# Kernel optimization log

Measured on AMD Instinct MI355X. Metric: run time of the kernel, lower is better.

The kernel has to match this reference:

```python
import jax, jax.numpy as jnp
import numpy as np


def setup_inputs() -> dict:
    key = jax.random.key(0)
    k1, k2 = jax.random.split(key)
    B, H, N, D = 4, 16, 2048, 64
    x = jax.random.normal(k1, (B, H, N, D), dtype=jnp.float32)
    wqkv = 0.02 * jax.random.normal(k2, (H, D, 3 * D), dtype=jnp.float32)
    bqkv = jnp.zeros((H, 1, 3 * D), dtype=jnp.float32)
    return {"x": x, "wqkv": wqkv, "bqkv": bqkv}


def reference(x, wqkv, bqkv):
    # x: [B, H, N, D]; wqkv: [H, D, 3D]; bqkv: [H, 1, 3D]
    B, H, N, D = x.shape
    scale = D ** (-0.5)
    qkv = jnp.einsum('bhnd,hde->bhne', x, wqkv) + bqkv  # [B,H,N,3D]
    # Faithful to torch: reshape (3D,) -> (D, 3) then unbind last axis,
    # i.e. q/k/v are interleaved (stride-3) columns of the projection.
    qkv = qkv.reshape(B, H, N, D, 3)
    q = qkv[..., 0] * scale
    k = qkv[..., 1]
    v = qkv[..., 2]
    attn = jnp.einsum('bhqd,bhkd->bhqk', q, k)  # [B,H,N,N]
    attn = jax.nn.softmax(attn, axis=-1)
    out = jnp.einsum('bhqk,bhkd->bhqd', attn, v)  # [B,H,N,D]
    return out
```

## Files before the change

kernel.cpp:

```cpp
#include <hip/hip_runtime.h>
#include <hip/hip_bf16.h>
#include <stdint.h>

typedef short bf16x8 __attribute__((ext_vector_type(8)));
typedef short bf16x4 __attribute__((ext_vector_type(4)));
typedef float f32x4 __attribute__((ext_vector_type(4)));

#define BHC 64
#define NQ 2048
#define DD 64
#define NE 192
#define LDP 72
#define WPS (64 * LDP + 8)
#define QSCALE 0.1803368801111245f

__device__ __forceinline__ short f2bf(float f) {
  unsigned u = __float_as_uint(f);
  unsigned r = (u + 0x7FFFu + ((u >> 16) & 1u)) >> 16;
  return (short)r;
}

__device__ __forceinline__ bf16x8 pack8(float4 a, float4 b) {
  bf16x8 v;
  v[0] = f2bf(a.x); v[1] = f2bf(a.y); v[2] = f2bf(a.z); v[3] = f2bf(a.w);
  v[4] = f2bf(b.x); v[5] = f2bf(b.y); v[6] = f2bf(b.z); v[7] = f2bf(b.w);
  return v;
}

__device__ __forceinline__ short2 pk_bf16(float a, float b) {
  __hip_bfloat162 c = __float22bfloat162_rn(make_float2(a, b));
  return *reinterpret_cast<short2*>(&c);
}

__global__ __launch_bounds__(256, 4) void proj_kernel(
    const float* __restrict__ x, const float* __restrict__ w,
    const float* __restrict__ bq, short* __restrict__ Qg,
    short* __restrict__ Kg, short* __restrict__ Vtg) {
  __shared__ short wt[3 * WPS];
  __shared__ short sV[4][64 * 24];

  const int tid = threadIdx.x;
  const int bh = blockIdx.x >> 5;
  const int rb = blockIdx.x & 31;
  const int h = bh & 15;

  const float* whp = w + (size_t)h * DD * NE;
  for (int i = 0; i < 48; ++i) {
    int idx = i * 256 + tid;
    int d = idx / NE, e = idx - d * NE;
    int dd = e / 3, wh = e - dd * 3;
    wt[wh * WPS + dd * LDP + d] = f2bf(whp[idx]);
  }
  __syncthreads();

  const int wave = tid >> 6;
  const int lane = tid & 63;
  const int col = lane & 15, quad = lane >> 4;
  const int row0 = rb * 64 + wave * 16;

  const float* xrow = x + ((size_t)bh * NQ + row0 + col) * DD;
  bf16x8 aq[2];
#pragma unroll
  for (int kc = 0; kc < 2; ++kc) {
    const float4* p4 = (const float4*)(xrow + kc * 32 + quad * 8);
    aq[kc] = pack8(p4[0], p4[1]);
  }

  f32x4 acc[12];
#pragma unroll
  for (int nt = 0; nt < 12; ++nt) acc[nt] = (f32x4){0.f, 0.f, 0.f, 0.f};

#pragma unroll
  for (int nt = 0; nt < 12; ++nt) {
    const short* wrow = &wt[(nt >> 2) * WPS + ((nt & 3) * 16 + col) * LDP];
#pragma unroll
    for (int kc = 0; kc < 2; ++kc) {
      bf16x8 bw = *(const bf16x8*)(wrow + kc * 32 + quad * 8);
      acc[nt] = __builtin_amdgcn_mfma_f32_16x16x32_bf16(aq[kc], bw, acc[nt], 0, 0, 0);
    }
  }

  const float* bqh = bq + h * NE;
  short* Qp = Qg + ((size_t)bh * NQ + row0) * DD;
  short* Kp = Kg + ((size_t)bh * NQ + row0) * DD;
  short* sVw = sV[wave];

#pragma unroll
  for (int nt = 0; nt < 12; ++nt) {
    int dd = (nt & 3) * 16 + col;
    float bias = bqh[dd * 3 + (nt >> 2)];
    float v0 = acc[nt][0] + bias, v1 = acc[nt][1] + bias;
    float v2 = acc[nt][2] + bias, v3 = acc[nt][3] + bias;
    if (nt < 4) { v0 *= QSCALE; v1 *= QSCALE; v2 *= QSCALE; v3 *= QSCALE; }
    short2 s01 = pk_bf16(v0, v1);
    short2 s23 = pk_bf16(v2, v3);
    int rowl = quad * 4;
    if (nt < 4) {
      Qp[rowl * DD + dd] = s01.x; Qp[(rowl + 1) * DD + dd] = s01.y;
      Qp[(rowl + 2) * DD + dd] = s23.x; Qp[(rowl + 3) * DD + dd] = s23.y;
    } else if (nt < 8) {
      Kp[rowl * DD + dd] = s01.x; Kp[(rowl + 1) * DD + dd] = s01.y;
      Kp[(rowl + 2) * DD + dd] = s23.x; Kp[(rowl + 3) * DD + dd] = s23.y;
    } else {
      sVw[dd * 24 + rowl] = s01.x; sVw[dd * 24 + rowl + 1] = s01.y;
      sVw[dd * 24 + rowl + 2] = s23.x; sVw[dd * 24 + rowl + 3] = s23.y;
    }
  }

  short* Vp = Vtg + (size_t)bh * DD * NQ + row0;
#pragma unroll
  for (int c = 0; c < 2; ++c) {
    int idx = c * 64 + lane;
    int d = idx >> 1, half = (idx & 1) * 8;
    *(bf16x8*)(Vp + (size_t)d * NQ + half) = *(const bf16x8*)(sVw + d * 24 + half);
  }
}

__global__ __launch_bounds__(256, 2) void attn_kernel(
    const short* __restrict__ Qg, const short* __restrict__ Kg,
    const short* __restrict__ Vtg, float* __restrict__ out) {
  __shared__ short kbuf[2][64 * 64];
  __shared__ short vbuf[2][64 * 64];
  __shared__ short pbuf[4][64 * LDP];

  const int tid = threadIdx.x;
  const int bh = blockIdx.x & 63;
  const int qb = blockIdx.x >> 6;
  const int wave = tid >> 6, lane = tid & 63;
  const int col = lane & 15, quad = lane >> 4;
  const int qbase = qb * 256 + wave * 64;

  bf16x8 bqf[4][2];
#pragma unroll
  for (int ntq = 0; ntq < 4; ++ntq)
#pragma unroll
    for (int kc = 0; kc < 2; ++kc)
      bqf[ntq][kc] = *(const bf16x8*)(Qg + ((size_t)bh * NQ + qbase + ntq * 16 + col) * DD +
                                      kc * 32 + quad * 8);

  f32x4 o[4][4];
  float l_acc[4];
#pragma unroll
  for (int mtq = 0; mtq < 4; ++mtq) {
    l_acc[mtq] = 0.f;
#pragma unroll
    for (int ntd = 0; ntd < 4; ++ntd) o[mtq][ntd] = (f32x4){0.f, 0.f, 0.f, 0.f};
  }

  short* pb = pbuf[wave];
  const short* Kb = Kg + (size_t)bh * NQ * DD;
  const short* Vb = Vtg + (size_t)bh * DD * NQ;

  const int r0 = tid >> 3, c0 = tid & 7;
  const int dst0 = r0 * 64 + ((c0 ^ (r0 & 7)) * 8);
  const int dst1 = (r0 + 32) * 64 + ((c0 ^ (r0 & 7)) * 8);
  const int src0 = r0 * DD + c0 * 8;
  const size_t vsrc0o = (size_t)r0 * NQ + c0 * 8;
  const size_t vsrc1o = (size_t)(r0 + 32) * NQ + c0 * 8;

  {
    bf16x8 k0 = *(const bf16x8*)(Kb + src0);
    bf16x8 k1 = *(const bf16x8*)(Kb + src0 + 32 * DD);
    bf16x8 v0 = *(const bf16x8*)(Vb + vsrc0o);
    bf16x8 v1 = *(const bf16x8*)(Vb + vsrc1o);
    *(bf16x8*)(&kbuf[0][dst0]) = k0;
    *(bf16x8*)(&kbuf[0][dst1]) = k1;
    *(bf16x8*)(&vbuf[0][dst0]) = v0;
    *(bf16x8*)(&vbuf[0][dst1]) = v1;
  }
  __syncthreads();

#pragma unroll 1
  for (int t = 0; t < 32; ++t) {
    const int p = t & 1;
    const short* kb = kbuf[p];
    const short* vb_s = vbuf[p];

    bf16x8 nk0, nk1, nv0, nv1;
    if (t < 31) {
      const short* Kn = Kb + (t + 1) * 64 * DD;
      const short* Vn = Vb + (t + 1) * 64;
      nk0 = *(const bf16x8*)(Kn + src0);
      nk1 = *(const bf16x8*)(Kn + src0 + 32 * DD);
      nv0 = *(const bf16x8*)(Vn + vsrc0o);
      nv1 = *(const bf16x8*)(Vn + vsrc1o);
    }

#pragma unroll
    for (int mtk = 0; mtk < 4; ++mtk) {
      const int krow = mtk * 16 + col;
      const int kx = krow & 7;
      bf16x8 ka0 = *(const bf16x8*)(&kb[krow * 64 + ((quad ^ kx) * 8)]);
      bf16x8 ka1 = *(const bf16x8*)(&kb[krow * 64 + (((4 + quad) ^ kx) * 8)]);
#pragma unroll
      for (int ntq = 0; ntq < 4; ++ntq) {
        f32x4 s = (f32x4){0.f, 0.f, 0.f, 0.f};
        s = __builtin_amdgcn_mfma_f32_16x16x32_bf16(ka0, bqf[ntq][0], s, 0, 0, 0);
        s = __builtin_amdgcn_mfma_f32_16x16x32_bf16(ka1, bqf[ntq][1], s, 0, 0, 0);
        float p0 = __builtin_amdgcn_exp2f(s[0]);
        float p1 = __builtin_amdgcn_exp2f(s[1]);
        float p2 = __builtin_amdgcn_exp2f(s[2]);
        float p3 = __builtin_amdgcn_exp2f(s[3]);
        l_acc[ntq] += (p0 + p1) + (p2 + p3);
        short2 s01 = pk_bf16(p0, p1);
        short2 s23 = pk_bf16(p2, p3);
        bf16x4 pv; pv[0] = s01.x; pv[1] = s01.y; pv[2] = s23.x; pv[3] = s23.y;
        *(bf16x4*)(&pb[(ntq * 16 + col) * LDP + mtk * 16 + quad * 4]) = pv;
      }
    }

#pragma unroll
    for (int mtq = 0; mtq < 4; ++mtq) {
      bf16x8 ap0 = *(const bf16x8*)(&pb[(mtq * 16 + col) * LDP + quad * 8]);
      bf16x8 ap1 = *(const bf16x8*)(&pb[(mtq * 16 + col) * LDP + 32 + quad * 8]);
#pragma unroll
      for (int ntd = 0; ntd < 4; ++ntd) {
        const int vrow = ntd * 16 + col;
        const int vx = vrow & 7;
        bf16x8 vf0 = *(const bf16x8*)(&vb_s[vrow * 64 + ((quad ^ vx) * 8)]);
        bf16x8 vf1 = *(const bf16x8*)(&vb_s[vrow * 64 + (((4 + quad) ^ vx) * 8)]);
        o[mtq][ntd] = __builtin_amdgcn_mfma_f32_16x16x32_bf16(ap0, vf0, o[mtq][ntd], 0, 0, 0);
        o[mtq][ntd] = __builtin_amdgcn_mfma_f32_16x16x32_bf16(ap1, vf1, o[mtq][ntd], 0, 0, 0);
      }
    }

    if (t < 31) {
      short* kn = kbuf[1 - p];
      short* vn = vbuf[1 - p];
      *(bf16x8*)(&kn[dst0]) = nk0;
      *(bf16x8*)(&kn[dst1]) = nk1;
      *(bf16x8*)(&vn[dst0]) = nv0;
      *(bf16x8*)(&vn[dst1]) = nv1;
      __syncthreads();
    }
  }

#pragma unroll
  for (int mtq = 0; mtq < 4; ++mtq) {
    float l = l_acc[mtq];
    l += __shfl_xor(l, 16);
    l += __shfl_xor(l, 32);
#pragma unroll
    for (int r = 0; r < 4; ++r) {
      float inv = 1.0f / __shfl(l, quad * 4 + r);
      int rq = qbase + mtq * 16 + quad * 4 + r;
      float* orow = out + ((size_t)bh * NQ + rq) * DD;
#pragma unroll
      for (int ntd = 0; ntd < 4; ++ntd) orow[ntd * 16 + col] = o[mtq][ntd][r] * inv;
    }
  }
}

extern "C" void kernel_launch(void* const* d_in, const int* in_sizes, int n_in,
                              void* d_out, int out_size, void* d_ws, size_t ws_size,
                              hipStream_t stream) {
  const float* x = (const float*)d_in[0];
  const float* w = (const float*)d_in[1];
  const float* bq = (const float*)d_in[2];
  float* out = (float*)d_out;

  short* Qg = (short*)d_ws;
  short* Kg = Qg + (size_t)BHC * NQ * DD;
  short* Vtg = Kg + (size_t)BHC * NQ * DD;

  proj_kernel<<<dim3(2048), dim3(256), 0, stream>>>(x, w, bq, Qg, Kg, Vtg);
  attn_kernel<<<dim3(512), dim3(256), 0, stream>>>(Qg, Kg, Vtg, out);
}
```

Measured before the change: 178.5 us.

## Pre-pack projection weights in MFMA fragment order via separate prep kernel

Adds a small kernel that converts the per-head QKV weights to bf16 once, already arranged in MFMA fragment order, and de-interleaves the bias. The projection kernel then loads weight fragments straight from global memory (L2-resident) instead of having each of 2048 blocks convert the full weight matrix into shared memory and synchronise. MFMA operands are swapped so each lane holds whole rows, which allows vectorized bf16x4 stores of Q and K. The cost is one extra kernel launch and weight reads from global or cache inside the MFMA loop rather than from LDS.

```diff
diff --git a/kernel.cpp b/kernel.cpp
--- a/kernel.cpp
+++ b/kernel.cpp
@@ -11,7 +11,6 @@
 #define DD 64
 #define NE 192
 #define LDP 72
-#define WPS (64 * LDP + 8)
 #define QSCALE 0.1803368801111245f
 
 __device__ __forceinline__ short f2bf(float f) {
@@ -32,27 +31,34 @@
   return *reinterpret_cast<short2*>(&c);
 }
 
+__global__ __launch_bounds__(256) void wprep_kernel(
+    const float* __restrict__ w, const float* __restrict__ bq,
+    short* __restrict__ wp, float* __restrict__ biasp) {
+  const int h = blockIdx.y;
+  const int r = blockIdx.x * 256 + threadIdx.x;
+  const int j = r & 7;
+  const int t = r >> 3;
+  const int quad = t & 3, col = (t >> 2) & 15;
+  const int kc = (t >> 6) & 1, ntb = (t >> 7) & 3, wh = t >> 9;
+  const int d = kc * 32 + quad * 8 + j;
+  const int e = (ntb * 16 + col) * 3 + wh;
+  wp[h * 12288 + r] = f2bf(w[((size_t)h * DD + d) * NE + e]);
+  if (r < 192) {
+    const int wh2 = r / 64, c = r - wh2 * 64;
+    biasp[h * 192 + r] = bq[h * NE + c * 3 + wh2];
+  }
+}
+
 __global__ __launch_bounds__(256, 4) void proj_kernel(
-    const float* __restrict__ x, const float* __restrict__ w,
-    const float* __restrict__ bq, short* __restrict__ Qg,
+    const float* __restrict__ x, const short* __restrict__ wp,
+    const float* __restrict__ biasp, short* __restrict__ Qg,
     short* __restrict__ Kg, short* __restrict__ Vtg) {
-  __shared__ short wt[3 * WPS];
   __shared__ short sV[4][64 * 24];
 
   const int tid = threadIdx.x;
   const int bh = blockIdx.x >> 5;
   const int rb = blockIdx.x & 31;
   const int h = bh & 15;
-
-  const float* whp = w + (size_t)h * DD * NE;
-  for (int i = 0; i < 48; ++i) {
-    int idx = i * 256 + tid;
-    int d = idx / NE, e = idx - d * NE;
-    int dd = e / 3, wh = e - dd * 3;
-    wt[wh * WPS + dd * LDP + d] = f2bf(whp[idx]);
-  }
-  __syncthreads();
-
   const int wave = tid >> 6;
   const int lane = tid & 63;
   const int col = lane & 15, quad = lane >> 4;
@@ -66,44 +72,45 @@
     aq[kc] = pack8(p4[0], p4[1]);
   }
 
+  const short* wph = wp + h * 12288;
+  const int fo = (col * 4 + quad) * 8;
+
   f32x4 acc[12];
 #pragma unroll
   for (int nt = 0; nt < 12; ++nt) acc[nt] = (f32x4){0.f, 0.f, 0.f, 0.f};
 
 #pragma unroll
   for (int nt = 0; nt < 12; ++nt) {
-    const short* wrow = &wt[(nt >> 2) * WPS + ((nt & 3) * 16 + col) * LDP];
-#pragma unroll
-    for (int kc = 0; kc < 2; ++kc) {
-      bf16x8 bw = *(const bf16x8*)(wrow + kc * 32 + quad * 8);
-      acc[nt] = __builtin_amdgcn_mfma_f32_16x16x32_bf16(aq[kc], bw, acc[nt], 0, 0, 0);
-    }
-  }
-
-  const float* bqh = bq + h * NE;
-  short* Qp = Qg + ((size_t)bh * NQ + row0) * DD;
-  short* Kp = Kg + ((size_t)bh * NQ + row0) * DD;
+    bf16x8 bw0 = *(const bf16x8*)(wph + (nt * 2 + 0) * 512 + fo);
+    bf16x8 bw1 = *(const bf16x8*)(wph + (nt * 2 + 1) * 512 + fo);
+    acc[nt] = __builtin_amdgcn_mfma_f32_16x16x32_bf16(bw0, aq[0], acc[nt], 0, 0, 0);
+    acc[nt] = __builtin_amdgcn_mfma_f32_16x16x32_bf16(bw1, aq[1], acc[nt], 0, 0, 0);
+  }
+
+  const float* bph = biasp + h * 192;
+  short* Qp = Qg + ((size_t)bh * NQ + row0 + col) * DD;
+  short* Kp = Kg + ((size_t)bh * NQ + row0 + col) * DD;
   short* sVw = sV[wave];
 
 #pragma unroll
   for (int nt = 0; nt < 12; ++nt) {
-    int dd = (nt & 3) * 16 + col;
-    float bias = bqh[dd * 3 + (nt >> 2)];
-    float v0 = acc[nt][0] + bias, v1 = acc[nt][1] + bias;
-    float v2 = acc[nt][2] + bias, v3 = acc[nt][3] + bias;
+    const int wh = nt >> 2, ntb = nt & 3;
+    const float4 b4 = *(const float4*)(bph + wh * 64 + ntb * 16 + quad * 4);
+    float v0 = acc[nt][0] + b4.x, v1 = acc[nt][1] + b4.y;
+    float v2 = acc[nt][2] + b4.z, v3 = acc[nt][3] + b4.w;
     if (nt < 4) { v0 *= QSCALE; v1 *= QSCALE; v2 *= QSCALE; v3 *= QSCALE; }
-    short2 s01 = pk_bf16(v0, v1);
-    short2 s23 = pk_bf16(v2, v3);
-    int rowl = quad * 4;
-    if (nt < 4) {
-      Qp[rowl * DD + dd] = s01.x; Qp[(rowl + 1) * DD + dd] = s01.y;
-      Qp[(rowl + 2) * DD + dd] = s23.x; Qp[(rowl + 3) * DD + dd] = s23.y;
-    } else if (nt < 8) {
-      Kp[rowl * DD + dd] = s01.x; Kp[(rowl + 1) * DD + dd] = s01.y;
-      Kp[(rowl + 2) * DD + dd] = s23.x; Kp[(rowl + 3) * DD + dd] = s23.y;
+    if (nt < 8) {
+      short2 s01 = pk_bf16(v0, v1);
+      short2 s23 = pk_bf16(v2, v3);
+      bf16x4 pv; pv[0] = s01.x; pv[1] = s01.y; pv[2] = s23.x; pv[3] = s23.y;
+      short* P = (nt < 4) ? Qp : Kp;
+      *(bf16x4*)(P + ntb * 16 + quad * 4) = pv;
     } else {
-      sVw[dd * 24 + rowl] = s01.x; sVw[dd * 24 + rowl + 1] = s01.y;
-      sVw[dd * 24 + rowl + 2] = s23.x; sVw[dd * 24 + rowl + 3] = s23.y;
+      const int dd = ntb * 16 + quad * 4;
+      sVw[(dd + 0) * 24 + col] = f2bf(v0);
+      sVw[(dd + 1) * 24 + col] = f2bf(v1);
+      sVw[(dd + 2) * 24 + col] = f2bf(v2);
+      sVw[(dd + 3) * 24 + col] = f2bf(v3);
     }
   }
 
@@ -262,7 +269,10 @@
   short* Qg = (short*)d_ws;
   short* Kg = Qg + (size_t)BHC * NQ * DD;
   short* Vtg = Kg + (size_t)BHC * NQ * DD;
-
-  proj_kernel<<<dim3(2048), dim3(256), 0, stream>>>(x, w, bq, Qg, Kg, Vtg);
+  short* wp = Vtg + (size_t)BHC * DD * NQ;
+  float* biasp = (float*)(wp + 16 * 12288);
+
+  wprep_kernel<<<dim3(48, 16), dim3(256), 0, stream>>>(w, bq, wp, biasp);
+  proj_kernel<<<dim3(2048), dim3(256), 0, stream>>>(x, wp, biasp, Qg, Kg, Vtg);
   attn_kernel<<<dim3(512), dim3(256), 0, stream>>>(Qg, Kg, Vtg, out);
 }
```

Measured after the change: 183.8 us. +3.0%, slower.
